# Kernel tuning notes

Hardware: AMD Instinct MI355X
Metric: run time of the kernel (lower is better)

Reference implementation:

```python
import jax, jax.numpy as jnp
from jax import lax
import numpy as np

COST_CLASS, COST_BOX, COST_GIOU = 1.0, 5.0, 2.0
B, Q, C, T = 16, 900, 92, 100
INF = jnp.float32(1e18)


def setup_inputs() -> dict:
    key = jax.random.key(0)
    k1, k2, k3, k4 = jax.random.split(key, 4)
    pred_logits = jax.random.normal(k1, (B, Q, C), jnp.float32)

    def mk_boxes(k, n):
        kc, ks = jax.random.split(k)
        cxcy = jax.random.uniform(kc, (B, n, 2), jnp.float32) * 0.8 + 0.1
        wh = jax.random.uniform(ks, (B, n, 2), jnp.float32) * 0.2 + 0.05
        return jnp.concatenate([cxcy, wh], axis=-1)  # valid cxcywh in (0,1)

    pred_boxes = mk_boxes(k2, Q)
    tgt_boxes = mk_boxes(k3, T)
    tgt_labels = jax.random.randint(k4, (B, T), 0, C)
    return {"pred_logits": pred_logits, "pred_boxes": pred_boxes,
            "tgt_labels": tgt_labels, "tgt_boxes": tgt_boxes}


def box_cxcywh_to_xyxy(b):
    cx, cy, w, h = b[..., 0], b[..., 1], b[..., 2], b[..., 3]
    return jnp.stack([cx - 0.5 * w, cy - 0.5 * h, cx + 0.5 * w, cy + 0.5 * h], axis=-1)


def generalized_box_iou(a, b):
    # a: [B,Q,4] xyxy, b: [B,T,4] xyxy -> [B,Q,T]
    area_a = (a[..., 2] - a[..., 0]) * (a[..., 3] - a[..., 1])  # [B,Q]
    area_b = (b[..., 2] - b[..., 0]) * (b[..., 3] - b[..., 1])  # [B,T]
    a_ = a[:, :, None, :]
    b_ = b[:, None, :, :]
    lt = jnp.maximum(a_[..., :2], b_[..., :2])
    rb = jnp.minimum(a_[..., 2:], b_[..., 2:])
    wh = jnp.clip(rb - lt, 0.0)
    inter = wh[..., 0] * wh[..., 1]
    union = area_a[:, :, None] + area_b[:, None, :] - inter
    iou = inter / union
    lt_c = jnp.minimum(a_[..., :2], b_[..., :2])
    rb_c = jnp.maximum(a_[..., 2:], b_[..., 2:])
    wh_c = jnp.clip(rb_c - lt_c, 0.0)
    area_c = wh_c[..., 0] * wh_c[..., 1]
    return iou - (area_c - union) / area_c


def cost_matrix(pred_logits, pred_boxes, tgt_labels, tgt_boxes):
    probs = jax.nn.softmax(pred_logits, axis=-1)                         # [B,Q,C]
    cost_class = -jnp.take_along_axis(probs, tgt_labels[:, None, :], 2)  # [B,Q,T]
    cost_box = jnp.abs(pred_boxes[:, :, None, :] - tgt_boxes[:, None, :, :]).sum(-1)
    cost_giou = -generalized_box_iou(box_cxcywh_to_xyxy(pred_boxes),
                                     box_cxcywh_to_xyxy(tgt_boxes))
    return COST_BOX * cost_box + COST_CLASS * cost_class + COST_GIOU * cost_giou


def hungarian(cost):
    # Jonker-Volgenant shortest augmenting path. cost: [n, m], n <= m, minimize.
    # Returns col_for_row [n]: column assigned to each row.
    n, m = cost.shape

    def solve_row(i, uvp):
        u, v, p = uvp  # u:[n+1] row potentials, v:[m+1] col potentials, p:[m+1] col->row (n = free)
        p = p.at[m].set(i)  # virtual start column holds current row
        minv = jnp.full((m,), INF, jnp.float32)
        way = jnp.zeros((m,), jnp.int32)
        used = jnp.zeros((m + 1,), bool)
        j0 = jnp.int32(m)

        def cond(s):
            _, _, _, _, _, j0 = s
            return p[j0] != n  # stop when a free column is reached

        def body(s):
            u, v, minv, way, used, j0 = s
            used = used.at[j0].set(True)
            i0 = p[j0]
            cur = cost[i0] - u[i0] - v[:m]           # reduced costs of row i0
            mask = (~used[:m]) & (cur < minv)
            minv = jnp.where(mask, cur, minv)
            way = jnp.where(mask, j0, way)
            mvals = jnp.where(used[:m], INF, minv)
            j1 = jnp.argmin(mvals).astype(jnp.int32)
            delta = mvals[j1]
            u = u.at[p].add(jnp.where(used, delta, 0.0))
            v = v - jnp.where(used, delta, 0.0)
            minv = jnp.where(used[:m], minv, minv - delta)
            return (u, v, minv, way, used, j1)

        u, v, minv, way, used, j0 = lax.while_loop(cond, body, (u, v, minv, way, used, j0))

        def acond(s):
            _, j0 = s
            return j0 != m

        def abody(s):
            p, j0 = s
            j1 = way[j0]
            p = p.at[j0].set(p[j1])
            return (p, j1)

        p, _ = lax.while_loop(acond, abody, (p, j0))
        return (u, v, p)

    u0 = jnp.zeros((n + 1,), jnp.float32)
    v0 = jnp.zeros((m + 1,), jnp.float32)
    p0 = jnp.full((m + 1,), n, jnp.int32)
    _, _, p = lax.fori_loop(0, n, solve_row, (u0, v0, p0))
    col_for_row = jnp.zeros((n + 1,), jnp.int32).at[p[:m]].set(
        jnp.arange(m, dtype=jnp.int32))[:n]
    return col_for_row


def reference(pred_logits, pred_boxes, tgt_labels, tgt_boxes):
    cost = cost_matrix(pred_logits, pred_boxes, tgt_labels, tgt_boxes)  # [B,Q,T]
    # assign each target (row) to a distinct query (col); vmap over batch
    q_per_t = jax.vmap(hungarian)(jnp.swapaxes(cost, 1, 2))  # [B,T]
    order = jnp.argsort(q_per_t, axis=-1)                    # sort by query idx (scipy convention)
    q_idx = jnp.take_along_axis(q_per_t, order, axis=-1)     # query indices  [B,T]
    t_idx = order.astype(jnp.int32)                          # target indices [B,T]
    return cost, q_idx, t_idx
```

## Files before the change

kernel.cpp:

```cpp
#include <hip/hip_runtime.h>

#define BB 16
#define QQ 900
#define QP 960
#define VIRT QP
#define CC 92
#define TT 100
#define INFF 1e18f
#define NK 15

#define DPP_STEP_F(x, ctrl, OP)                                             \
  do {                                                                      \
    float _o = __int_as_float(__builtin_amdgcn_update_dpp(                  \
        __float_as_int(x), __float_as_int(x), (ctrl), 0xF, 0xF, false));    \
    (x) = OP((x), _o);                                                      \
  } while (0)

__device__ __forceinline__ float wave_fmax63(float x) {
  DPP_STEP_F(x, 0xB1, fmaxf);
  DPP_STEP_F(x, 0x4E, fmaxf);
  DPP_STEP_F(x, 0x141, fmaxf);
  DPP_STEP_F(x, 0x140, fmaxf);
  DPP_STEP_F(x, 0x142, fmaxf);
  DPP_STEP_F(x, 0x143, fmaxf);
  return x;
}
__device__ __forceinline__ float wave_fmin63(float x) {
  DPP_STEP_F(x, 0xB1, fminf);
  DPP_STEP_F(x, 0x4E, fminf);
  DPP_STEP_F(x, 0x141, fminf);
  DPP_STEP_F(x, 0x140, fminf);
  DPP_STEP_F(x, 0x142, fminf);
  DPP_STEP_F(x, 0x143, fminf);
  return x;
}
__device__ __forceinline__ float wave_fadd63(float x) {
#define ADDF(a, b) ((a) + (b))
  DPP_STEP_F(x, 0xB1, ADDF);
  DPP_STEP_F(x, 0x4E, ADDF);
  DPP_STEP_F(x, 0x141, ADDF);
  DPP_STEP_F(x, 0x140, ADDF);
  DPP_STEP_F(x, 0x142, ADDF);
  DPP_STEP_F(x, 0x143, ADDF);
#undef ADDF
  return x;
}
__device__ __forceinline__ int wave_imin63(int x) {
  {int _o=__builtin_amdgcn_update_dpp(x,x,0xB1,0xF,0xF,false); x=_o<x?_o:x;}
  {int _o=__builtin_amdgcn_update_dpp(x,x,0x4E,0xF,0xF,false); x=_o<x?_o:x;}
  {int _o=__builtin_amdgcn_update_dpp(x,x,0x141,0xF,0xF,false);x=_o<x?_o:x;}
  {int _o=__builtin_amdgcn_update_dpp(x,x,0x140,0xF,0xF,false);x=_o<x?_o:x;}
  {int _o=__builtin_amdgcn_update_dpp(x,x,0x142,0xF,0xF,false);x=_o<x?_o:x;}
  {int _o=__builtin_amdgcn_update_dpp(x,x,0x143,0xF,0xF,false);x=_o<x?_o:x;}
  return x;
}

#define KEY_STEP(CTRL)                                                      \
  do {                                                                      \
    unsigned olo = (unsigned)__builtin_amdgcn_update_dpp(                   \
        (int)klo, (int)klo, (CTRL), 0xF, 0xF, false);                       \
    unsigned ohi = (unsigned)__builtin_amdgcn_update_dpp(                   \
        (int)khi, (int)khi, (CTRL), 0xF, 0xF, false);                       \
    const unsigned long long cur8 =                                         \
        ((unsigned long long)khi << 32) | klo;                              \
    const unsigned long long oth8 =                                         \
        ((unsigned long long)ohi << 32) | olo;                              \
    if (oth8 < cur8) { khi = ohi; klo = olo; }                              \
  } while (0)

__device__ __forceinline__ void stage_row(const float* __restrict__ row,
                                          float* buf, int lane) {
  typedef __attribute__((address_space(1))) const void gv_t;
  typedef __attribute__((address_space(3))) void lv_t;
  __builtin_amdgcn_global_load_lds((gv_t*)(row + lane * 4),       (lv_t*)(buf),       16, 0, 0);
  __builtin_amdgcn_global_load_lds((gv_t*)(row + 256 + lane * 4), (lv_t*)(buf + 256), 16, 0, 0);
  __builtin_amdgcn_global_load_lds((gv_t*)(row + 512 + lane * 4), (lv_t*)(buf + 512), 16, 0, 0);
  __builtin_amdgcn_global_load_lds((gv_t*)(row + 768 + lane),     (lv_t*)(buf + 768), 4, 0, 0);
  __builtin_amdgcn_global_load_lds((gv_t*)(row + 832 + lane),     (lv_t*)(buf + 832), 4, 0, 0);
  __builtin_amdgcn_global_load_lds((gv_t*)(row + 896 + lane),     (lv_t*)(buf + 896), 4, 0, 0);
}

__device__ __forceinline__ int p_get(unsigned a, unsigned b, unsigned c,
                                     unsigned d, int j) {
  const int l = j & 63, kq = j >> 6;
  unsigned r0 = (unsigned)__builtin_amdgcn_readlane((int)a, l);
  unsigned r1 = (unsigned)__builtin_amdgcn_readlane((int)b, l);
  unsigned r2 = (unsigned)__builtin_amdgcn_readlane((int)c, l);
  unsigned r3 = (unsigned)__builtin_amdgcn_readlane((int)d, l);
  unsigned r = (kq < 8) ? (kq < 4 ? r0 : r1) : (kq < 12 ? r2 : r3);
  return (int)((r >> ((kq & 3) * 8)) & 0xFFu);
}

#define P_SET(jj, val)                                                      \
  do {                                                                      \
    const int _j = (jj); const int _kq = _j >> 6;                           \
    const unsigned _sh = (unsigned)((_kq & 3) * 8);                         \
    const unsigned _nm = ~(0xFFu << _sh);                                   \
    const unsigned _in = ((unsigned)(val) & 0xFFu) << _sh;                  \
    const bool _own = (lane == (_j & 63));                                  \
    if (_kq < 4)       { if (_own) p4a = (p4a & _nm) | _in; }               \
    else if (_kq < 8)  { if (_own) p4b = (p4b & _nm) | _in; }               \
    else if (_kq < 12) { if (_own) p4c = (p4c & _nm) | _in; }               \
    else               { if (_own) p4d = (p4d & _nm) | _in; }               \
  } while (0)

__global__ __launch_bounds__(64) void cost_kernel(
    const float* __restrict__ logits,
    const float* __restrict__ pboxes,
    const int*   __restrict__ tlabels,
    const float* __restrict__ tboxes,
    float* __restrict__ cost,
    float* __restrict__ costT,
    int ctp)
{
  const int bq   = blockIdx.x;
  const int b    = bq / QQ;
  const int q    = bq - b * QQ;
  const int lane = threadIdx.x;

  __shared__ float sl[CC];

  const float a = logits[(size_t)bq * CC + lane];
  const float bb2 = (lane < CC - 64)
                        ? logits[(size_t)bq * CC + 64 + lane]
                        : -3.402823466e38f;

  float mx = fmaxf(a, bb2);
  mx = wave_fmax63(mx);
  const float m = __int_as_float(
      __builtin_amdgcn_readlane(__float_as_int(mx), 63));

  const float e0 = expf(a - m);
  const float e1 = (lane < CC - 64) ? expf(bb2 - m) : 0.0f;
  sl[lane] = e0;
  if (lane < CC - 64) sl[64 + lane] = e1;

  float sm = e0 + e1;
  sm = wave_fadd63(sm);
  const float ssum = __int_as_float(
      __builtin_amdgcn_readlane(__float_as_int(sm), 63));

  const float4 pbv = ((const float4*)pboxes)[bq];
  const float pax1 = pbv.x - 0.5f * pbv.z, pay1 = pbv.y - 0.5f * pbv.w;
  const float pax2 = pbv.x + 0.5f * pbv.z, pay2 = pbv.y + 0.5f * pbv.w;
  const float area_a = (pax2 - pax1) * (pay2 - pay1);

  for (int t = lane; t < TT; t += 64) {
    const int lab = tlabels[b * TT + t];
    const float cc = -(sl[lab] / ssum);

    const float4 tb = ((const float4*)tboxes)[b * TT + t];
    const float cbox = fabsf(pbv.x - tb.x) + fabsf(pbv.y - tb.y) +
                       fabsf(pbv.z - tb.z) + fabsf(pbv.w - tb.w);

    const float bx1 = tb.x - 0.5f * tb.z, by1 = tb.y - 0.5f * tb.w;
    const float bx2 = tb.x + 0.5f * tb.z, by2 = tb.y + 0.5f * tb.w;
    const float area_b = (bx2 - bx1) * (by2 - by1);

    const float ltx = fmaxf(pax1, bx1), lty = fmaxf(pay1, by1);
    const float rbx = fminf(pax2, bx2), rby = fminf(pay2, by2);
    const float iw = fmaxf(rbx - ltx, 0.0f), ih = fmaxf(rby - lty, 0.0f);
    const float inter = iw * ih;
    const float uni = area_a + area_b - inter;
    const float iou = inter / uni;

    const float cx1 = fminf(pax1, bx1), cy1 = fminf(pay1, by1);
    const float cx2 = fmaxf(pax2, bx2), cy2 = fmaxf(pay2, by2);
    const float cw = fmaxf(cx2 - cx1, 0.0f), ch = fmaxf(cy2 - cy1, 0.0f);
    const float ac = cw * ch;
    const float giou = iou - (ac - uni) / ac;

    const float cval = 5.0f * cbox + cc - 2.0f * giou;
    cost[(size_t)bq * TT + t] = cval;
    if (ctp) costT[((size_t)b * TT + t) * ctp + q] = cval;
  }
  if (ctp == QP && q < QP - QQ) {
    for (int t = lane; t < TT; t += 64)
      costT[((size_t)b * TT + t) * QP + QQ + q] = INFF;
  }
}

__global__ void __launch_bounds__(64)
hungarianT_kernel(
    const float* __restrict__ ct,
    float* __restrict__ out_q,
    float* __restrict__ out_t)
{
  const int b    = blockIdx.x;
  const int lane = threadIdx.x;

  __shared__ __align__(16) float rowbuf[QP];
  __shared__ int way_lds[QP];
  __shared__ int qpt[TT];

  const float* __restrict__ base = ct + (size_t)b * TT * QP;

#pragma unroll
  for (int k = 0; k < NK; ++k) way_lds[k * 64 + lane] = -1;

  unsigned p4a = 0x64646464u, p4b = 0x64646464u;
  unsigned p4c = 0x64646464u, p4d = 0x64646464u;

  float u0 = 0.0f, u1 = 0.0f;
  float v[NK];
#pragma unroll
  for (int k = 0; k < NK; ++k) v[k] = 0.0f;

  stage_row(base, &rowbuf[0], lane);

  for (int i = 0; i < TT; ++i) {
    asm volatile("s_waitcnt vmcnt(0)" ::: "memory");
    float c[NK];
#pragma unroll
    for (int k = 0; k < NK; ++k) c[k] = rowbuf[k * 64 + lane];
    asm volatile("s_waitcnt lgkmcnt(0)" ::: "memory");
    if (i + 1 < TT) stage_row(base + (size_t)(i + 1) * QP, &rowbuf[0], lane);

    float minv[NK];
#pragma unroll
    for (int k = 0; k < NK; ++k) minv[k] = INFF;
    unsigned umask = 0;
    const int stamp = i << 12;

    int i0 = i;
    int j0 = VIRT;
    int jfin;

    float us = (i0 < 64) ? u0 : u1;
    float ui0 = __int_as_float(
        __builtin_amdgcn_readlane(__float_as_int(us), i0 & 63));

    for (int step = 0; step < 128; ++step) {
      if (i0 == lane)      umask |= (1u << 30);
      if (i0 == 64 + lane) umask |= (1u << 31);
      if (j0 != VIRT && (j0 & 63) == lane) umask |= (1u << (j0 >> 6));

      const bool dowrite = (j0 != VIRT);

      float lmin  = INFF;
      int   kbest = 0;
#pragma unroll
      for (int k = 0; k < NK; ++k) {
        const bool  uk  = (umask >> k) & 1u;
        const float cur = c[k] - ui0 - v[k];
        const bool  imp = !uk && (cur < minv[k]);
        if (imp) {
          minv[k] = cur;
          if (dowrite) way_lds[k * 64 + lane] = stamp | j0;
        }
        const float eff = uk ? INFF : minv[k];
        if (eff < lmin) { lmin = eff; kbest = k; }
      }
      const int lidx = (kbest << 6) + lane;

      unsigned fb = __float_as_uint(lmin);
      fb = (fb & 0x80000000u) ? ~fb : (fb | 0x80000000u);
      unsigned khi = fb, klo = (unsigned)lidx;
      KEY_STEP(0xB1);
      KEY_STEP(0x4E);
      KEY_STEP(0x141);
      KEY_STEP(0x140);
      KEY_STEP(0x142);
      KEY_STEP(0x143);
      const int j1 = __builtin_amdgcn_readlane((int)klo, 63);
      const unsigned hb =
          (unsigned)__builtin_amdgcn_readlane((int)khi, 63);
      const float delta =
          __uint_as_float((hb & 0x80000000u) ? (hb ^ 0x80000000u) : ~hb);

      const int  i0n = p_get(p4a, p4b, p4c, p4d, j1);
      const bool fin = (i0n == TT);

      if (!fin) {
        const float* __restrict__ prow = base + (size_t)i0n * QP;
#pragma unroll
        for (int k = 0; k < NK; ++k) c[k] = prow[k * 64 + lane];
      }

      u0 += ((umask >> 30) & 1u) ? delta : 0.0f;
      u1 += (umask >> 31)        ? delta : 0.0f;
#pragma unroll
      for (int k = 0; k < NK; ++k)
        v[k] -= ((umask >> k) & 1u) ? delta : 0.0f;
      if (!fin) {
#pragma unroll
        for (int k = 0; k < NK; ++k)
          minv[k] -= ((umask >> k) & 1u) ? 0.0f : delta;
      }

      if (fin) { jfin = j1; break; }
      float us2 = (i0n < 64) ? u0 : u1;
      ui0 = __int_as_float(
          __builtin_amdgcn_readlane(__float_as_int(us2), i0n & 63));
      j0 = j1;
      i0 = i0n;
    }

    if (j0 == VIRT) {
      P_SET(jfin, i);
    } else {
      int j = jfin;
      for (int hop = 0; hop < 128 && j != VIRT; ++hop) {
        int raw = way_lds[j];
        raw = __builtin_amdgcn_readfirstlane(raw);
        const int jn = ((raw >> 12) == i) ? (raw & 0xFFF) : VIRT;
        const int pj = (jn == VIRT) ? i : p_get(p4a, p4b, p4c, p4d, jn);
        P_SET(j, pj);
        j = jn;
      }
    }
  }

#pragma unroll
  for (int k = 0; k < NK; ++k) {
    const unsigned reg = (k < 4) ? p4a : (k < 8) ? p4b : (k < 12) ? p4c : p4d;
    const int r = (int)((reg >> ((k & 3) * 8)) & 0xFFu);
    const int j = k * 64 + lane;
    if (r < TT) qpt[r] = j;
  }
  __syncthreads();

  for (int t = lane; t < TT; t += 64) {
    const int myq = qpt[t];
    int rank = 0;
    for (int t2 = 0; t2 < TT; ++t2) rank += (qpt[t2] < myq) ? 1 : 0;
    out_q[b * TT + rank] = (float)myq;
    out_t[b * TT + rank] = (float)t;
  }
}

__global__ void __launch_bounds__(64)
hungarian_kernel(
    const float* __restrict__ cost,
    const float* __restrict__ costT,
    float* __restrict__ out_q,
    float* __restrict__ out_t)
{
  const int b    = blockIdx.x;
  const int lane = threadIdx.x;

  __shared__ int p_lds[QQ + 1];
  __shared__ int way_lds[QQ];
  __shared__ int qpt[TT];

  const float* base;
  size_t rs, cs;
  if (costT) { base = costT + (size_t)b * TT * QQ; rs = QQ; cs = 1; }
  else       { base = cost  + (size_t)b * QQ * TT; rs = 1;  cs = TT; }

  for (int j = lane; j <= QQ; j += 64) p_lds[j] = TT;

  float u0 = 0.0f, u1 = 0.0f;
  float v[NK];
#pragma unroll
  for (int k = 0; k < NK; ++k) v[k] = 0.0f;

  float c[NK];
#pragma unroll
  for (int k = 0; k < NK; ++k) {
    const int j = k * 64 + lane;
    c[k] = (j < QQ) ? base[(size_t)j * cs] : 0.0f;
  }

  for (int i = 0; i < TT; ++i) {
    p_lds[QQ] = i;

    float minv[NK];
#pragma unroll
    for (int k = 0; k < NK; ++k) minv[k] = INFF;
    unsigned umask = 0;
    bool t0 = false, t1 = false;

    int i0 = i;
    int j0 = QQ;
    int jfin;

    float us = (i0 < 64) ? u0 : u1;
    float ui0 = __int_as_float(
        __builtin_amdgcn_readlane(__float_as_int(us), i0 & 63));

    while (true) {
      t0 = t0 || (i0 == lane);
      t1 = t1 || (i0 == 64 + lane);
      if (j0 != QQ) {
        if ((j0 & 63) == lane) umask |= (1u << (j0 >> 6));
      }

      float lmin = INFF;
      int   lidx = QQ;
#pragma unroll
      for (int k = 0; k < NK; ++k) {
        const int j = k * 64 + lane;
        if (j < QQ && !((umask >> k) & 1u)) {
          const float cur = c[k] - ui0 - v[k];
          if (cur < minv[k]) { minv[k] = cur; way_lds[j] = j0; }
          if (minv[k] < lmin) { lmin = minv[k]; lidx = j; }
        }
      }

      float red = wave_fmin63(lmin);
      const float delta = __int_as_float(
          __builtin_amdgcn_readlane(__float_as_int(red), 63));
      int cand = (lmin == delta) ? lidx : 0x7FFFFFFF;
      int redi = wave_imin63(cand);
      const int j1 = __builtin_amdgcn_readlane(redi, 63);

      int i0n = p_lds[j1];
      i0n = __builtin_amdgcn_readfirstlane(i0n);
      const bool fin = (i0n == TT);

      u0 += t0 ? delta : 0.0f;
      u1 += t1 ? delta : 0.0f;
#pragma unroll
      for (int k = 0; k < NK; ++k) {
        const bool uk = (umask >> k) & 1u;
        v[k]    -= uk ? delta : 0.0f;
        minv[k] -= uk ? 0.0f  : delta;
      }

      if (!fin) {
        float us2 = (i0n < 64) ? u0 : u1;
        ui0 = __int_as_float(
            __builtin_amdgcn_readlane(__float_as_int(us2), i0n & 63));
#pragma unroll
        for (int k = 0; k < NK; ++k) {
          const int j = k * 64 + lane;
          if (j < QQ) c[k] = base[(size_t)i0n * rs + (size_t)j * cs];
        }
      }
      asm volatile("" ::: "memory");

      if (fin) { jfin = j1; break; }
      j0 = j1;
      i0 = i0n;
    }

    if (i + 1 < TT) {
#pragma unroll
      for (int k = 0; k < NK; ++k) {
        const int jj = k * 64 + lane;
        if (jj < QQ) c[k] = base[(size_t)(i + 1) * rs + (size_t)jj * cs];
      }
    }

    int j = jfin;
    while (j != QQ) {
      const int jn = way_lds[j];
      const int pj = p_lds[jn];
      p_lds[j] = pj;
      j = jn;
    }
    asm volatile("" ::: "memory");
  }

#pragma unroll
  for (int k = 0; k < NK; ++k) {
    const int j = k * 64 + lane;
    if (j < QQ) {
      const int r = p_lds[j];
      if (r < TT) qpt[r] = j;
    }
  }
  __syncthreads();

  for (int t = lane; t < TT; t += 64) {
    const int myq = qpt[t];
    int rank = 0;
    for (int t2 = 0; t2 < TT; ++t2) rank += (qpt[t2] < myq) ? 1 : 0;
    out_q[b * TT + rank] = (float)myq;
    out_t[b * TT + rank] = (float)t;
  }
}

extern "C" void kernel_launch(void* const* d_in, const int* in_sizes, int n_in,
                              void* d_out, int out_size, void* d_ws, size_t ws_size,
                              hipStream_t stream) {
  const float* logits  = (const float*)d_in[0];
  const float* pboxes  = (const float*)d_in[1];
  const int*   tlabels = (const int*)d_in[2];
  const float* tboxes  = (const float*)d_in[3];

  float* out  = (float*)d_out;
  float* cost = out;
  float* oq   = out + (size_t)BB * QQ * TT;
  float* ot   = oq + (size_t)BB * TT;

  const size_t padded_bytes = (size_t)BB * TT * QP * sizeof(float);
  const size_t plain_bytes  = (size_t)BB * TT * QQ * sizeof(float);

  if (ws_size >= padded_bytes) {
    float* costT = (float*)d_ws;
    hipLaunchKernelGGL(cost_kernel, dim3(BB * QQ), dim3(64), 0, stream,
                       logits, pboxes, tlabels, tboxes, cost, costT, QP);
    hipLaunchKernelGGL(hungarianT_kernel, dim3(BB), dim3(64), 0, stream,
                       costT, oq, ot);
  } else if (ws_size >= plain_bytes) {
    float* costT = (float*)d_ws;
    hipLaunchKernelGGL(cost_kernel, dim3(BB * QQ), dim3(64), 0, stream,
                       logits, pboxes, tlabels, tboxes, cost, costT, QQ);
    hipLaunchKernelGGL(hungarian_kernel, dim3(BB), dim3(64), 0, stream,
                       cost, costT, oq, ot);
  } else {
    hipLaunchKernelGGL(cost_kernel, dim3(BB * QQ), dim3(64), 0, stream,
                       logits, pboxes, tlabels, tboxes, cost, (float*)nullptr, 0);
    hipLaunchKernelGGL(hungarian_kernel, dim3(BB), dim3(64), 0, stream,
                       cost, (const float*)nullptr, oq, ot);
  }
}
```

Baseline: 215.9 us.

## Prefetch next cost row into registers and simplify argmin wave reduction

Drops the LDS staging buffer that used global_load_lds. The next row is now loaded straight into registers during the first augmentation step, or after the path search when the search took more than one step. The packed 64-bit DPP key reduction is replaced by a float-min DPP reduction, followed by a ballot and readlane to recover the argmin column. This shortens the serial per-step critical path. Tie-breaking now favours the lowest lane rather than the lowest column index, and the early prefetch is wasted whenever the search takes more than one step.

```diff
diff --git a/kernel.cpp b/kernel.cpp
--- a/kernel.cpp
+++ b/kernel.cpp
@@ -53,31 +53,6 @@
   {int _o=__builtin_amdgcn_update_dpp(x,x,0x142,0xF,0xF,false);x=_o<x?_o:x;}
   {int _o=__builtin_amdgcn_update_dpp(x,x,0x143,0xF,0xF,false);x=_o<x?_o:x;}
   return x;
-}
-
-#define KEY_STEP(CTRL)                                                      \
-  do {                                                                      \
-    unsigned olo = (unsigned)__builtin_amdgcn_update_dpp(                   \
-        (int)klo, (int)klo, (CTRL), 0xF, 0xF, false);                       \
-    unsigned ohi = (unsigned)__builtin_amdgcn_update_dpp(                   \
-        (int)khi, (int)khi, (CTRL), 0xF, 0xF, false);                       \
-    const unsigned long long cur8 =                                         \
-        ((unsigned long long)khi << 32) | klo;                              \
-    const unsigned long long oth8 =                                         \
-        ((unsigned long long)ohi << 32) | olo;                              \
-    if (oth8 < cur8) { khi = ohi; klo = olo; }                              \
-  } while (0)
-
-__device__ __forceinline__ void stage_row(const float* __restrict__ row,
-                                          float* buf, int lane) {
-  typedef __attribute__((address_space(1))) const void gv_t;
-  typedef __attribute__((address_space(3))) void lv_t;
-  __builtin_amdgcn_global_load_lds((gv_t*)(row + lane * 4),       (lv_t*)(buf),       16, 0, 0);
-  __builtin_amdgcn_global_load_lds((gv_t*)(row + 256 + lane * 4), (lv_t*)(buf + 256), 16, 0, 0);
-  __builtin_amdgcn_global_load_lds((gv_t*)(row + 512 + lane * 4), (lv_t*)(buf + 512), 16, 0, 0);
-  __builtin_amdgcn_global_load_lds((gv_t*)(row + 768 + lane),     (lv_t*)(buf + 768), 4, 0, 0);
-  __builtin_amdgcn_global_load_lds((gv_t*)(row + 832 + lane),     (lv_t*)(buf + 832), 4, 0, 0);
-  __builtin_amdgcn_global_load_lds((gv_t*)(row + 896 + lane),     (lv_t*)(buf + 896), 4, 0, 0);
 }
 
 __device__ __forceinline__ int p_get(unsigned a, unsigned b, unsigned c,
@@ -189,7 +164,6 @@
   const int b    = blockIdx.x;
   const int lane = threadIdx.x;
 
-  __shared__ __align__(16) float rowbuf[QP];
   __shared__ int way_lds[QP];
   __shared__ int qpt[TT];
 
@@ -206,16 +180,11 @@
 #pragma unroll
   for (int k = 0; k < NK; ++k) v[k] = 0.0f;
 
-  stage_row(base, &rowbuf[0], lane);
+  float c[NK];
+#pragma unroll
+  for (int k = 0; k < NK; ++k) c[k] = base[k * 64 + lane];
 
   for (int i = 0; i < TT; ++i) {
-    asm volatile("s_waitcnt vmcnt(0)" ::: "memory");
-    float c[NK];
-#pragma unroll
-    for (int k = 0; k < NK; ++k) c[k] = rowbuf[k * 64 + lane];
-    asm volatile("s_waitcnt lgkmcnt(0)" ::: "memory");
-    if (i + 1 < TT) stage_row(base + (size_t)(i + 1) * QP, &rowbuf[0], lane);
-
     float minv[NK];
 #pragma unroll
     for (int k = 0; k < NK; ++k) minv[k] = INFF;
@@ -231,11 +200,10 @@
         __builtin_amdgcn_readlane(__float_as_int(us), i0 & 63));
 
     for (int step = 0; step < 128; ++step) {
+      const bool first = (j0 == VIRT);
       if (i0 == lane)      umask |= (1u << 30);
       if (i0 == 64 + lane) umask |= (1u << 31);
-      if (j0 != VIRT && (j0 & 63) == lane) umask |= (1u << (j0 >> 6));
-
-      const bool dowrite = (j0 != VIRT);
+      if (!first && (j0 & 63) == lane) umask |= (1u << (j0 >> 6));
 
       float lmin  = INFF;
       int   kbest = 0;
@@ -246,27 +214,25 @@
         const bool  imp = !uk && (cur < minv[k]);
         if (imp) {
           minv[k] = cur;
-          if (dowrite) way_lds[k * 64 + lane] = stamp | j0;
+          if (!first) way_lds[k * 64 + lane] = stamp | j0;
         }
         const float eff = uk ? INFF : minv[k];
         if (eff < lmin) { lmin = eff; kbest = k; }
       }
       const int lidx = (kbest << 6) + lane;
 
-      unsigned fb = __float_as_uint(lmin);
-      fb = (fb & 0x80000000u) ? ~fb : (fb | 0x80000000u);
-      unsigned khi = fb, klo = (unsigned)lidx;
-      KEY_STEP(0xB1);
-      KEY_STEP(0x4E);
-      KEY_STEP(0x141);
-      KEY_STEP(0x140);
-      KEY_STEP(0x142);
-      KEY_STEP(0x143);
-      const int j1 = __builtin_amdgcn_readlane((int)klo, 63);
-      const unsigned hb =
-          (unsigned)__builtin_amdgcn_readlane((int)khi, 63);
-      const float delta =
-          __uint_as_float((hb & 0x80000000u) ? (hb ^ 0x80000000u) : ~hb);
+      if (first && i + 1 < TT) {
+        const float* __restrict__ nrow = base + (size_t)(i + 1) * QP;
+#pragma unroll
+        for (int k = 0; k < NK; ++k) c[k] = nrow[k * 64 + lane];
+      }
+
+      float red = wave_fmin63(lmin);
+      const float delta = __int_as_float(
+          __builtin_amdgcn_readlane(__float_as_int(red), 63));
+      const unsigned long long bmask = __ballot(lmin == delta);
+      const int wl = (int)(__ffsll((long long)bmask) - 1);
+      const int j1 = __builtin_amdgcn_readlane(lidx, wl);
 
       const int  i0n = p_get(p4a, p4b, p4c, p4d, j1);
       const bool fin = (i0n == TT);
@@ -287,6 +253,7 @@
         for (int k = 0; k < NK; ++k)
           minv[k] -= ((umask >> k) & 1u) ? 0.0f : delta;
       }
+      asm volatile("" ::: "memory");
 
       if (fin) { jfin = j1; break; }
       float us2 = (i0n < 64) ? u0 : u1;
@@ -296,7 +263,15 @@
       i0 = i0n;
     }
 
-    if (j0 == VIRT) {
+    const bool single = (j0 == VIRT);
+
+    if (!single && i + 1 < TT) {
+      const float* __restrict__ nrow = base + (size_t)(i + 1) * QP;
+#pragma unroll
+      for (int k = 0; k < NK; ++k) c[k] = nrow[k * 64 + lane];
+    }
+
+    if (single) {
       P_SET(jfin, i);
     } else {
       int j = jfin;
@@ -309,6 +284,7 @@
         j = jn;
       }
     }
+    asm volatile("" ::: "memory");
   }
 
 #pragma unroll
```

New measurement: 200.2 us. 1.08x faster.
